# Optimization experiments

Measured on AMD Instinct MI355X. Metric: run time of the kernel, lower is better.

Reference implementation:

```python
import jax, jax.numpy as jnp
import numpy as np

N_USERS = 100000
EMBED = 128
N_EDGES = 1_600_000  # avg degree 16


def setup_inputs() -> dict:
    key = jax.random.key(0)
    k1, k2, k3, k4, k5 = jax.random.split(key, 5)
    s_rows = jnp.sort(jax.random.randint(k1, (N_EDGES,), 0, N_USERS))
    s_cols = jax.random.randint(k2, (N_EDGES,), 0, N_USERS)
    # row-normalization D^-1 A, matching the scipy preprocessing in __init__
    deg = jax.ops.segment_sum(jnp.ones((N_EDGES,), jnp.float32), s_rows, num_segments=N_USERS)
    deg = jnp.where(deg == 0, 1.0, deg)
    s_values = 1.0 / deg[s_rows]
    user_embeds = jax.random.normal(k3, (N_USERS, EMBED), jnp.float32) * 0.1
    bound = float(np.sqrt(6.0 / (EMBED + EMBED)))  # xavier_uniform
    W0 = jax.random.uniform(k4, (EMBED, EMBED), jnp.float32, -bound, bound)
    W1 = jax.random.uniform(k5, (EMBED, EMBED), jnp.float32, -bound, bound)
    return {"user_embeds": user_embeds, "s_rows": s_rows, "s_cols": s_cols,
            "s_values": s_values, "W0": W0, "W1": W1}


def reference(user_embeds, s_rows, s_cols, s_values, W0, W1):
    # SocialGCN.forward: per layer x_new = x + dropout(S @ (x @ W_l));
    # dropout is identity in eval mode. Returns all layer outputs (stacked).
    n_users = user_embeds.shape[0]
    outs = [user_embeds]
    x = user_embeds
    for W in (W0, W1):
        xt = x @ W  # [n_users, d] dense GEMM
        # SpMM: out[r] = sum_{e: rows[e]==r} vals[e] * xt[cols[e]]
        msg = s_values[:, None] * xt[s_cols]  # [n_edges, d] irregular gather
        agg = jax.ops.segment_sum(msg, s_rows, num_segments=n_users)
        x = x + agg  # residual add
        outs.append(x)
    return jnp.stack(outs)  # [n_layers+1, n_users, d]
```

## Files before the change

### kernel.cpp

```cpp
#include <hip/hip_runtime.h>

#define N_USERS  100000
#define EMBED    128

typedef __attribute__((ext_vector_type(8))) short bf16x8;
typedef __attribute__((ext_vector_type(4))) float f32x4;

__global__ __launch_bounds__(256) void rowptr_kernel(const int* __restrict__ rows,
                                                     int* __restrict__ row_ptr,
                                                     int n_rows, int n_edges) {
  int r = blockIdx.x * blockDim.x + threadIdx.x;
  if (r > n_rows) return;
  int lo = 0, hi = n_edges;
  while (lo < hi) {
    int mid = (lo + hi) >> 1;
    if (rows[mid] < r) lo = mid + 1; else hi = mid;
  }
  row_ptr[r] = lo;
}

__global__ __launch_bounds__(256) void wconv_kernel(const float* __restrict__ W0,
                                                    const float* __restrict__ W1,
                                                    uint* __restrict__ Wt0,
                                                    uint* __restrict__ Wt1) {
  const float* W  = blockIdx.x ? W1 : W0;
  uint*        Wt = blockIdx.x ? Wt1 : Wt0;
  for (int idx = threadIdx.x; idx < 128 * 64; idx += 256) {
    int n = idx >> 6;
    int kp = idx & 63;
    float a = W[(2 * kp) * 128 + n];
    float b = W[(2 * kp + 1) * 128 + n];
    uint o;
    asm("v_cvt_pk_bf16_f32 %0, %1, %2" : "=v"(o) : "v"(a), "v"(b));
    Wt[n * 64 + kp] = o;
  }
}

__global__ __launch_bounds__(256) void gemm_kernel(const float* __restrict__ X,
                                                   const ushort* __restrict__ Wt,
                                                   unsigned char* __restrict__ Y8,
                                                   float* __restrict__ scale_arr,
                                                   float* __restrict__ Xcopy) {
  const int tid  = threadIdx.x;
  const int wave = tid >> 6;
  const int lane = tid & 63;
  const int l15  = lane & 15;
  const int lg   = lane >> 4;
  const int m    = blockIdx.x * 64 + wave * 16 + l15;
  const int mc   = m < N_USERS ? m : N_USERS - 1;
  const bool act = m < N_USERS;
  const float* xrow = X + (size_t)mc * EMBED;

  f32x4 acc[8];
  #pragma unroll
  for (int t = 0; t < 8; ++t) acc[t] = (f32x4){0.f, 0.f, 0.f, 0.f};

  #pragma unroll
  for (int s = 0; s < 4; ++s) {
    const int k0 = s * 32 + lg * 8;
    float4 xa = *(const float4*)(xrow + k0);
    float4 xb = *(const float4*)(xrow + k0 + 4);
    if (Xcopy && act) {
      *(float4*)(Xcopy + (size_t)m * EMBED + k0)     = xa;
      *(float4*)(Xcopy + (size_t)m * EMBED + k0 + 4) = xb;
    }
    union { bf16x8 v; uint u[4]; } bfr;
    asm("v_cvt_pk_bf16_f32 %0, %1, %2" : "=v"(bfr.u[0]) : "v"(xa.x), "v"(xa.y));
    asm("v_cvt_pk_bf16_f32 %0, %1, %2" : "=v"(bfr.u[1]) : "v"(xa.z), "v"(xa.w));
    asm("v_cvt_pk_bf16_f32 %0, %1, %2" : "=v"(bfr.u[2]) : "v"(xb.x), "v"(xb.y));
    asm("v_cvt_pk_bf16_f32 %0, %1, %2" : "=v"(bfr.u[3]) : "v"(xb.z), "v"(xb.w));
    #pragma unroll
    for (int nt = 0; nt < 8; ++nt) {
      union { bf16x8 v; uint4 u; } afr;
      afr.u = *(const uint4*)(Wt + (size_t)(nt * 16 + l15) * 128 + k0);
      acc[nt] = __builtin_amdgcn_mfma_f32_16x16x32_bf16(afr.v, bfr.v, acc[nt], 0, 0, 0);
    }
  }

  if (act) {
    float amax = 0.f;
    #pragma unroll
    for (int nt = 0; nt < 8; ++nt)
      #pragma unroll
      for (int i = 0; i < 4; ++i) amax = fmaxf(amax, fabsf(acc[nt][i]));
    amax = fmaxf(amax, __shfl_xor(amax, 16));
    amax = fmaxf(amax, __shfl_xor(amax, 32));
    const float inv = amax > 0.f ? 127.0f / amax : 0.f;
    if (lg == 0) scale_arr[m] = amax * (1.0f / 127.0f);

    unsigned char* yrow = Y8 + (size_t)m * EMBED;
    #pragma unroll
    for (int nt = 0; nt < 8; ++nt) {
      uint q = 0;
      #pragma unroll
      for (int i = 0; i < 4; ++i) {
        int qi = __float2int_rn(acc[nt][i] * inv) + 128;
        q |= (uint)qi << (8 * i);
      }
      *(uint*)(yrow + nt * 16 + lg * 4) = q;
    }
  }
}

__device__ __forceinline__ void fma8b(float* a, uint2 g, float vs) {
  float f;
  #define CVT_ACC(word, b, slot)                                        \
    asm("v_cvt_f32_ubyte" #b " %0, %1" : "=v"(f) : "v"(word));          \
    a[slot] = fmaf(vs, f, a[slot]);
  CVT_ACC(g.x, 0, 0) CVT_ACC(g.x, 1, 1) CVT_ACC(g.x, 2, 2) CVT_ACC(g.x, 3, 3)
  CVT_ACC(g.y, 0, 4) CVT_ACC(g.y, 1, 5) CVT_ACC(g.y, 2, 6) CVT_ACC(g.y, 3, 7)
  #undef CVT_ACC
}

__global__ __launch_bounds__(256) void spmm_fused_kernel(
    const unsigned char* __restrict__ XT8, const float* __restrict__ scale_in,
    const float* __restrict__ X, const int* __restrict__ row_ptr,
    const int* __restrict__ cols, const float* __restrict__ vals,
    const ushort* __restrict__ Wt, float* __restrict__ OUT,
    unsigned char* __restrict__ Y8, float* __restrict__ scale_out) {
  const int tid  = threadIdx.x;
  const int wave = tid >> 6;
  const int lane = tid & 63;
  const int l15  = lane & 15;
  const int lg   = lane >> 4;
  const int row  = blockIdx.x * 64 + wave * 16 + l15;
  const int rowc = row < N_USERS ? row : N_USERS - 1;
  const bool act = row < N_USERS;
  const int start = row_ptr[rowc];
  const int end   = row_ptr[rowc + 1];

  float acc[4][8];
  #pragma unroll
  for (int s = 0; s < 4; ++s)
    #pragma unroll
    for (int j = 0; j < 8; ++j) acc[s][j] = 0.f;
  float vsum = 0.f;

  const uint2* base2 = (const uint2*)XT8;
  int e = start;
  int e_pre = (start + 3) & ~3;
  if (e_pre > end) e_pre = end;
  for (; e < e_pre; ++e) {
    int c = cols[e];
    float vs = vals[e] * scale_in[c];
    vsum += vs;
    const uint2* src = base2 + (size_t)c * 16 + lg;
    uint2 g0 = src[0], g1 = src[4], g2 = src[8], g3 = src[12];
    fma8b(acc[0], g0, vs); fma8b(acc[1], g1, vs);
    fma8b(acc[2], g2, vs); fma8b(acc[3], g3, vs);
  }
  for (; e + 4 <= end; e += 4) {
    int4   ca = *(const int4*)(cols + e);
    float4 va = *(const float4*)(vals + e);
    float vs0 = va.x * scale_in[ca.x], vs1 = va.y * scale_in[ca.y];
    float vs2 = va.z * scale_in[ca.z], vs3 = va.w * scale_in[ca.w];
    vsum += vs0 + vs1 + vs2 + vs3;
    const uint2* s0 = base2 + (size_t)ca.x * 16 + lg;
    const uint2* s1 = base2 + (size_t)ca.y * 16 + lg;
    const uint2* s2 = base2 + (size_t)ca.z * 16 + lg;
    const uint2* s3 = base2 + (size_t)ca.w * 16 + lg;
    uint2 a0 = s0[0], a1 = s0[4], a2 = s0[8],  a3 = s0[12];
    uint2 b0 = s1[0], b1 = s1[4], b2 = s1[8],  b3 = s1[12];
    uint2 c0 = s2[0], c1 = s2[4], c2 = s2[8],  c3 = s2[12];
    uint2 d0 = s3[0], d1 = s3[4], d2 = s3[8],  d3 = s3[12];
    fma8b(acc[0], a0, vs0); fma8b(acc[1], a1, vs0);
    fma8b(acc[2], a2, vs0); fma8b(acc[3], a3, vs0);
    fma8b(acc[0], b0, vs1); fma8b(acc[1], b1, vs1);
    fma8b(acc[2], b2, vs1); fma8b(acc[3], b3, vs1);
    fma8b(acc[0], c0, vs2); fma8b(acc[1], c1, vs2);
    fma8b(acc[2], c2, vs2); fma8b(acc[3], c3, vs2);
    fma8b(acc[0], d0, vs3); fma8b(acc[1], d1, vs3);
    fma8b(acc[2], d2, vs3); fma8b(acc[3], d3, vs3);
  }
  for (; e < end; ++e) {
    int c = cols[e];
    float vs = vals[e] * scale_in[c];
    vsum += vs;
    const uint2* src = base2 + (size_t)c * 16 + lg;
    uint2 g0 = src[0], g1 = src[4], g2 = src[8], g3 = src[12];
    fma8b(acc[0], g0, vs); fma8b(acc[1], g1, vs);
    fma8b(acc[2], g2, vs); fma8b(acc[3], g3, vs);
  }

  const float corr = vsum * 128.0f;
  union { bf16x8 v; uint4 u; } bfr[4];
  #pragma unroll
  for (int s = 0; s < 4; ++s) {
    const float* xr = X + (size_t)rowc * EMBED + s * 32 + lg * 8;
    float4 ra = *(const float4*)xr;
    float4 rb = *(const float4*)(xr + 4);
    float o0 = acc[s][0] - corr + ra.x, o1 = acc[s][1] - corr + ra.y;
    float o2 = acc[s][2] - corr + ra.z, o3 = acc[s][3] - corr + ra.w;
    float o4 = acc[s][4] - corr + rb.x, o5 = acc[s][5] - corr + rb.y;
    float o6 = acc[s][6] - corr + rb.z, o7 = acc[s][7] - corr + rb.w;
    if (act) {
      float* orow = OUT + (size_t)row * EMBED + s * 32 + lg * 8;
      *(float4*)orow       = (float4){o0, o1, o2, o3};
      *(float4*)(orow + 4) = (float4){o4, o5, o6, o7};
    }
    asm("v_cvt_pk_bf16_f32 %0, %1, %2" : "=v"(bfr[s].u.x) : "v"(o0), "v"(o1));
    asm("v_cvt_pk_bf16_f32 %0, %1, %2" : "=v"(bfr[s].u.y) : "v"(o2), "v"(o3));
    asm("v_cvt_pk_bf16_f32 %0, %1, %2" : "=v"(bfr[s].u.z) : "v"(o4), "v"(o5));
    asm("v_cvt_pk_bf16_f32 %0, %1, %2" : "=v"(bfr[s].u.w) : "v"(o6), "v"(o7));
  }

  f32x4 accg[8];
  #pragma unroll
  for (int t = 0; t < 8; ++t) accg[t] = (f32x4){0.f, 0.f, 0.f, 0.f};
  #pragma unroll
  for (int s = 0; s < 4; ++s) {
    const int k0 = s * 32 + lg * 8;
    #pragma unroll
    for (int nt = 0; nt < 8; ++nt) {
      union { bf16x8 v; uint4 u; } afr;
      afr.u = *(const uint4*)(Wt + (size_t)(nt * 16 + l15) * 128 + k0);
      accg[nt] = __builtin_amdgcn_mfma_f32_16x16x32_bf16(afr.v, bfr[s].v, accg[nt], 0, 0, 0);
    }
  }

  if (act) {
    float amax = 0.f;
    #pragma unroll
    for (int nt = 0; nt < 8; ++nt)
      #pragma unroll
      for (int i = 0; i < 4; ++i) amax = fmaxf(amax, fabsf(accg[nt][i]));
    amax = fmaxf(amax, __shfl_xor(amax, 16));
    amax = fmaxf(amax, __shfl_xor(amax, 32));
    const float inv = amax > 0.f ? 127.0f / amax : 0.f;
    if (lg == 0) scale_out[row] = amax * (1.0f / 127.0f);

    unsigned char* yrow = Y8 + (size_t)row * EMBED;
    #pragma unroll
    for (int nt = 0; nt < 8; ++nt) {
      uint q = 0;
      #pragma unroll
      for (int i = 0; i < 4; ++i) {
        int qi = __float2int_rn(accg[nt][i] * inv) + 128;
        q |= (uint)qi << (8 * i);
      }
      *(uint*)(yrow + nt * 16 + lg * 4) = q;
    }
  }
}

__device__ __forceinline__ void fma16(float* acc, uint4 g, float vs) {
  float f;
  #define CVT_ACC(word, b, slot)                                        \
    asm("v_cvt_f32_ubyte" #b " %0, %1" : "=v"(f) : "v"(word));          \
    acc[slot] = fmaf(vs, f, acc[slot]);
  CVT_ACC(g.x, 0, 0)  CVT_ACC(g.x, 1, 1)  CVT_ACC(g.x, 2, 2)  CVT_ACC(g.x, 3, 3)
  CVT_ACC(g.y, 0, 4)  CVT_ACC(g.y, 1, 5)  CVT_ACC(g.y, 2, 6)  CVT_ACC(g.y, 3, 7)
  CVT_ACC(g.z, 0, 8)  CVT_ACC(g.z, 1, 9)  CVT_ACC(g.z, 2, 10) CVT_ACC(g.z, 3, 11)
  CVT_ACC(g.w, 0, 12) CVT_ACC(g.w, 1, 13) CVT_ACC(g.w, 2, 14) CVT_ACC(g.w, 3, 15)
  #undef CVT_ACC
}

__global__ __launch_bounds__(256) void spmm_kernel(const unsigned char* __restrict__ XT8,
                                                   const float* __restrict__ scale_arr,
                                                   const float* __restrict__ X,
                                                   const int* __restrict__ row_ptr,
                                                   const int* __restrict__ cols,
                                                   const float* __restrict__ vals,
                                                   float* __restrict__ OUT) {
  const int tid = threadIdx.x;
  const int l   = tid & 7;
  const int rg  = tid >> 3;
  const int row = blockIdx.x * 32 + rg;
  if (row >= N_USERS) return;
  const int start = row_ptr[row];
  const int end   = row_ptr[row + 1];
  const uint4* XT4 = (const uint4*)XT8;

  float acc[16];
  #pragma unroll
  for (int j = 0; j < 16; ++j) acc[j] = 0.f;
  float vsum = 0.f;

  int e = start;
  int e_pre = (start + 3) & ~3;
  if (e_pre > end) e_pre = end;
  for (; e < e_pre; ++e) {
    int c = cols[e];
    float vs = vals[e] * scale_arr[c];
    vsum += vs;
    fma16(acc, XT4[(size_t)c * 8 + l], vs);
  }
  for (; e + 4 <= end; e += 4) {
    int4   ca = *(const int4*)(cols + e);
    float4 va = *(const float4*)(vals + e);
    float vs0 = va.x * scale_arr[ca.x], vs1 = va.y * scale_arr[ca.y];
    float vs2 = va.z * scale_arr[ca.z], vs3 = va.w * scale_arr[ca.w];
    uint4 g0 = XT4[(size_t)ca.x * 8 + l];
    uint4 g1 = XT4[(size_t)ca.y * 8 + l];
    uint4 g2 = XT4[(size_t)ca.z * 8 + l];
    uint4 g3 = XT4[(size_t)ca.w * 8 + l];
    vsum += vs0 + vs1 + vs2 + vs3;
    fma16(acc, g0, vs0);
    fma16(acc, g1, vs1);
    fma16(acc, g2, vs2);
    fma16(acc, g3, vs3);
  }
  for (; e < end; ++e) {
    int c = cols[e];
    float vs = vals[e] * scale_arr[c];
    vsum += vs;
    fma16(acc, XT4[(size_t)c * 8 + l], vs);
  }

  const float corr = vsum * 128.0f;
  const float* xr = X + (size_t)row * EMBED + l * 16;
  float*       orow = OUT + (size_t)row * EMBED + l * 16;
  #pragma unroll
  for (int k = 0; k < 4; ++k) {
    float4 r = *(const float4*)(xr + k * 4);
    float4 o = {acc[k * 4 + 0] - corr + r.x,
                acc[k * 4 + 1] - corr + r.y,
                acc[k * 4 + 2] - corr + r.z,
                acc[k * 4 + 3] - corr + r.w};
    *(float4*)(orow + k * 4) = o;
  }
}

extern "C" void kernel_launch(void* const* d_in, const int* in_sizes, int n_in,
                              void* d_out, int out_size, void* d_ws, size_t ws_size,
                              hipStream_t stream) {
  const float* user_embeds = (const float*)d_in[0];
  const int*   s_rows      = (const int*)d_in[1];
  const int*   s_cols      = (const int*)d_in[2];
  const float* s_values    = (const float*)d_in[3];
  const float* W0          = (const float*)d_in[4];
  const float* W1          = (const float*)d_in[5];
  float* out = (float*)d_out;

  const int n_edges = in_sizes[1];
  const size_t layer = (size_t)N_USERS * EMBED;

  char* ws = (char*)d_ws;
  unsigned char* xt8a = (unsigned char*)ws;  ws += layer;
  unsigned char* xt8b = (unsigned char*)ws;  ws += layer;
  float*  scale_a = (float*)ws;              ws += N_USERS * sizeof(float);
  float*  scale_b = (float*)ws;              ws += N_USERS * sizeof(float);
  ushort* Wt0     = (ushort*)ws;             ws += 128 * 128 * sizeof(ushort);
  ushort* Wt1     = (ushort*)ws;             ws += 128 * 128 * sizeof(ushort);
  int*    row_ptr = (int*)ws;

  rowptr_kernel<<<(N_USERS + 1 + 255) / 256, 256, 0, stream>>>(
      s_rows, row_ptr, N_USERS, n_edges);
  wconv_kernel<<<2, 256, 0, stream>>>(W0, W1, (uint*)Wt0, (uint*)Wt1);

  gemm_kernel<<<(N_USERS + 63) / 64, 256, 0, stream>>>(
      user_embeds, Wt0, xt8a, scale_a, out);
  spmm_fused_kernel<<<(N_USERS + 63) / 64, 256, 0, stream>>>(
      xt8a, scale_a, user_embeds, row_ptr, s_cols, s_values, Wt1,
      out + layer, xt8b, scale_b);
  spmm_kernel<<<(N_USERS + 31) / 32, 256, 0, stream>>>(
      xt8b, scale_b, out + layer, row_ptr, s_cols, s_values, out + 2 * layer);
}
```

Baseline: 226.5 us.

## Permute int8 embedding layout so SpMM gathers use 16-byte loads

The quantized XT8 rows are now written in a permuted order, so each lane in the fused SpMM kernel reads its 32 bytes per neighbor with two contiguous uint4 loads instead of four strided uint2 loads. The consumer kernels (fused and final SpMM) are updated to map output columns to that permuted layout. The fused kernel also reuses one accumulator union for both the aggregation and the MFMA stages and adds a min-blocks occupancy hint of 4. This aims to cut gather instruction count and register pressure, with the risk that any layout mismatch between writers and readers produces wrong results.

```diff
diff --git a/kernel.cpp b/kernel.cpp
--- a/kernel.cpp
+++ b/kernel.cpp
@@ -5,6 +5,7 @@
 
 typedef __attribute__((ext_vector_type(8))) short bf16x8;
 typedef __attribute__((ext_vector_type(4))) float f32x4;
+
 
 __global__ __launch_bounds__(256) void rowptr_kernel(const int* __restrict__ rows,
                                                      int* __restrict__ row_ptr,
@@ -88,7 +89,7 @@
     const float inv = amax > 0.f ? 127.0f / amax : 0.f;
     if (lg == 0) scale_arr[m] = amax * (1.0f / 127.0f);
 
-    unsigned char* yrow = Y8 + (size_t)m * EMBED;
+    uint* yrow = (uint*)(Y8 + (size_t)m * EMBED);
     #pragma unroll
     for (int nt = 0; nt < 8; ++nt) {
       uint q = 0;
@@ -97,22 +98,22 @@
         int qi = __float2int_rn(acc[nt][i] * inv) + 128;
         q |= (uint)qi << (8 * i);
       }
-      *(uint*)(yrow + nt * 16 + lg * 4) = q;
-    }
-  }
-}
-
-__device__ __forceinline__ void fma8b(float* a, uint2 g, float vs) {
+      yrow[(((nt & 1) << 1) | (lg >> 1)) * 8 + (nt >> 1) * 2 + (lg & 1)] = q;
+    }
+  }
+}
+
+__device__ __forceinline__ void fma8b(float* a, uint w0, uint w1, float vs) {
   float f;
   #define CVT_ACC(word, b, slot)                                        \
     asm("v_cvt_f32_ubyte" #b " %0, %1" : "=v"(f) : "v"(word));          \
     a[slot] = fmaf(vs, f, a[slot]);
-  CVT_ACC(g.x, 0, 0) CVT_ACC(g.x, 1, 1) CVT_ACC(g.x, 2, 2) CVT_ACC(g.x, 3, 3)
-  CVT_ACC(g.y, 0, 4) CVT_ACC(g.y, 1, 5) CVT_ACC(g.y, 2, 6) CVT_ACC(g.y, 3, 7)
+  CVT_ACC(w0, 0, 0) CVT_ACC(w0, 1, 1) CVT_ACC(w0, 2, 2) CVT_ACC(w0, 3, 3)
+  CVT_ACC(w1, 0, 4) CVT_ACC(w1, 1, 5) CVT_ACC(w1, 2, 6) CVT_ACC(w1, 3, 7)
   #undef CVT_ACC
 }
 
-__global__ __launch_bounds__(256) void spmm_fused_kernel(
+__global__ __launch_bounds__(256, 4) void spmm_fused_kernel(
     const unsigned char* __restrict__ XT8, const float* __restrict__ scale_in,
     const float* __restrict__ X, const int* __restrict__ row_ptr,
     const int* __restrict__ cols, const float* __restrict__ vals,
@@ -129,14 +130,12 @@
   const int start = row_ptr[rowc];
   const int end   = row_ptr[rowc + 1];
 
-  float acc[4][8];
-  #pragma unroll
-  for (int s = 0; s < 4; ++s)
-    #pragma unroll
-    for (int j = 0; j < 8; ++j) acc[s][j] = 0.f;
+  union AccU { float f[4][8]; f32x4 v[8]; } U;
+  #pragma unroll
+  for (int t = 0; t < 8; ++t) U.v[t] = (f32x4){0.f, 0.f, 0.f, 0.f};
   float vsum = 0.f;
 
-  const uint2* base2 = (const uint2*)XT8;
+  const uint4* B8 = (const uint4*)XT8;
   int e = start;
   int e_pre = (start + 3) & ~3;
   if (e_pre > end) e_pre = end;
@@ -144,10 +143,10 @@
     int c = cols[e];
     float vs = vals[e] * scale_in[c];
     vsum += vs;
-    const uint2* src = base2 + (size_t)c * 16 + lg;
-    uint2 g0 = src[0], g1 = src[4], g2 = src[8], g3 = src[12];
-    fma8b(acc[0], g0, vs); fma8b(acc[1], g1, vs);
-    fma8b(acc[2], g2, vs); fma8b(acc[3], g3, vs);
+    uint4 ga = B8[(size_t)c * 8 + lg * 2];
+    uint4 gb = B8[(size_t)c * 8 + lg * 2 + 1];
+    fma8b(U.f[0], ga.x, ga.y, vs); fma8b(U.f[1], ga.z, ga.w, vs);
+    fma8b(U.f[2], gb.x, gb.y, vs); fma8b(U.f[3], gb.z, gb.w, vs);
   }
   for (; e + 4 <= end; e += 4) {
     int4   ca = *(const int4*)(cols + e);
@@ -155,31 +154,27 @@
     float vs0 = va.x * scale_in[ca.x], vs1 = va.y * scale_in[ca.y];
     float vs2 = va.z * scale_in[ca.z], vs3 = va.w * scale_in[ca.w];
     vsum += vs0 + vs1 + vs2 + vs3;
-    const uint2* s0 = base2 + (size_t)ca.x * 16 + lg;
-    const uint2* s1 = base2 + (size_t)ca.y * 16 + lg;
-    const uint2* s2 = base2 + (size_t)ca.z * 16 + lg;
-    const uint2* s3 = base2 + (size_t)ca.w * 16 + lg;
-    uint2 a0 = s0[0], a1 = s0[4], a2 = s0[8],  a3 = s0[12];
-    uint2 b0 = s1[0], b1 = s1[4], b2 = s1[8],  b3 = s1[12];
-    uint2 c0 = s2[0], c1 = s2[4], c2 = s2[8],  c3 = s2[12];
-    uint2 d0 = s3[0], d1 = s3[4], d2 = s3[8],  d3 = s3[12];
-    fma8b(acc[0], a0, vs0); fma8b(acc[1], a1, vs0);
-    fma8b(acc[2], a2, vs0); fma8b(acc[3], a3, vs0);
-    fma8b(acc[0], b0, vs1); fma8b(acc[1], b1, vs1);
-    fma8b(acc[2], b2, vs1); fma8b(acc[3], b3, vs1);
-    fma8b(acc[0], c0, vs2); fma8b(acc[1], c1, vs2);
-    fma8b(acc[2], c2, vs2); fma8b(acc[3], c3, vs2);
-    fma8b(acc[0], d0, vs3); fma8b(acc[1], d1, vs3);
-    fma8b(acc[2], d2, vs3); fma8b(acc[3], d3, vs3);
+    uint4 a0 = B8[(size_t)ca.x * 8 + lg * 2], a1 = B8[(size_t)ca.x * 8 + lg * 2 + 1];
+    uint4 b0 = B8[(size_t)ca.y * 8 + lg * 2], b1 = B8[(size_t)ca.y * 8 + lg * 2 + 1];
+    uint4 c0 = B8[(size_t)ca.z * 8 + lg * 2], c1 = B8[(size_t)ca.z * 8 + lg * 2 + 1];
+    uint4 d0 = B8[(size_t)ca.w * 8 + lg * 2], d1 = B8[(size_t)ca.w * 8 + lg * 2 + 1];
+    fma8b(U.f[0], a0.x, a0.y, vs0); fma8b(U.f[1], a0.z, a0.w, vs0);
+    fma8b(U.f[2], a1.x, a1.y, vs0); fma8b(U.f[3], a1.z, a1.w, vs0);
+    fma8b(U.f[0], b0.x, b0.y, vs1); fma8b(U.f[1], b0.z, b0.w, vs1);
+    fma8b(U.f[2], b1.x, b1.y, vs1); fma8b(U.f[3], b1.z, b1.w, vs1);
+    fma8b(U.f[0], c0.x, c0.y, vs2); fma8b(U.f[1], c0.z, c0.w, vs2);
+    fma8b(U.f[2], c1.x, c1.y, vs2); fma8b(U.f[3], c1.z, c1.w, vs2);
+    fma8b(U.f[0], d0.x, d0.y, vs3); fma8b(U.f[1], d0.z, d0.w, vs3);
+    fma8b(U.f[2], d1.x, d1.y, vs3); fma8b(U.f[3], d1.z, d1.w, vs3);
   }
   for (; e < end; ++e) {
     int c = cols[e];
     float vs = vals[e] * scale_in[c];
     vsum += vs;
-    const uint2* src = base2 + (size_t)c * 16 + lg;
-    uint2 g0 = src[0], g1 = src[4], g2 = src[8], g3 = src[12];
-    fma8b(acc[0], g0, vs); fma8b(acc[1], g1, vs);
-    fma8b(acc[2], g2, vs); fma8b(acc[3], g3, vs);
+    uint4 ga = B8[(size_t)c * 8 + lg * 2];
+    uint4 gb = B8[(size_t)c * 8 + lg * 2 + 1];
+    fma8b(U.f[0], ga.x, ga.y, vs); fma8b(U.f[1], ga.z, ga.w, vs);
+    fma8b(U.f[2], gb.x, gb.y, vs); fma8b(U.f[3], gb.z, gb.w, vs);
   }
 
   const float corr = vsum * 128.0f;
@@ -189,10 +184,10 @@
     const float* xr = X + (size_t)rowc * EMBED + s * 32 + lg * 8;
     float4 ra = *(const float4*)xr;
     float4 rb = *(const float4*)(xr + 4);
-    float o0 = acc[s][0] - corr + ra.x, o1 = acc[s][1] - corr + ra.y;
-    float o2 = acc[s][2] - corr + ra.z, o3 = acc[s][3] - corr + ra.w;
-    float o4 = acc[s][4] - corr + rb.x, o5 = acc[s][5] - corr + rb.y;
-    float o6 = acc[s][6] - corr + rb.z, o7 = acc[s][7] - corr + rb.w;
+    float o0 = U.f[s][0] - corr + ra.x, o1 = U.f[s][1] - corr + ra.y;
+    float o2 = U.f[s][2] - corr + ra.z, o3 = U.f[s][3] - corr + ra.w;
+    float o4 = U.f[s][4] - corr + rb.x, o5 = U.f[s][5] - corr + rb.y;
+    float o6 = U.f[s][6] - corr + rb.z, o7 = U.f[s][7] - corr + rb.w;
     if (act) {
       float* orow = OUT + (size_t)row * EMBED + s * 32 + lg * 8;
       *(float4*)orow       = (float4){o0, o1, o2, o3};
@@ -204,9 +199,8 @@
     asm("v_cvt_pk_bf16_f32 %0, %1, %2" : "=v"(bfr[s].u.w) : "v"(o6), "v"(o7));
   }
 
-  f32x4 accg[8];
-  #pragma unroll
-  for (int t = 0; t < 8; ++t) accg[t] = (f32x4){0.f, 0.f, 0.f, 0.f};
+  #pragma unroll
+  for (int t = 0; t < 8; ++t) U.v[t] = (f32x4){0.f, 0.f, 0.f, 0.f};
   #pragma unroll
   for (int s = 0; s < 4; ++s) {
     const int k0 = s * 32 + lg * 8;
@@ -214,7 +208,7 @@
     for (int nt = 0; nt < 8; ++nt) {
       union { bf16x8 v; uint4 u; } afr;
       afr.u = *(const uint4*)(Wt + (size_t)(nt * 16 + l15) * 128 + k0);
-      accg[nt] = __builtin_amdgcn_mfma_f32_16x16x32_bf16(afr.v, bfr[s].v, accg[nt], 0, 0, 0);
+      U.v[nt] = __builtin_amdgcn_mfma_f32_16x16x32_bf16(afr.v, bfr[s].v, U.v[nt], 0, 0, 0);
     }
   }
 
@@ -223,22 +217,22 @@
     #pragma unroll
     for (int nt = 0; nt < 8; ++nt)
       #pragma unroll
-      for (int i = 0; i < 4; ++i) amax = fmaxf(amax, fabsf(accg[nt][i]));
+      for (int i = 0; i < 4; ++i) amax = fmaxf(amax, fabsf(U.v[nt][i]));
     amax = fmaxf(amax, __shfl_xor(amax, 16));
     amax = fmaxf(amax, __shfl_xor(amax, 32));
     const float inv = amax > 0.f ? 127.0f / amax : 0.f;
     if (lg == 0) scale_out[row] = amax * (1.0f / 127.0f);
 
-    unsigned char* yrow = Y8 + (size_t)row * EMBED;
+    uint* yrow = (uint*)(Y8 + (size_t)row * EMBED);
     #pragma unroll
     for (int nt = 0; nt < 8; ++nt) {
       uint q = 0;
       #pragma unroll
       for (int i = 0; i < 4; ++i) {
-        int qi = __float2int_rn(accg[nt][i] * inv) + 128;
+        int qi = __float2int_rn(U.v[nt][i] * inv) + 128;
         q |= (uint)qi << (8 * i);
       }
-      *(uint*)(yrow + nt * 16 + lg * 4) = q;
+      yrow[(((nt & 1) << 1) | (lg >> 1)) * 8 + (nt >> 1) * 2 + (lg & 1)] = q;
     }
   }
 }
@@ -308,17 +302,21 @@
   }
 
   const float corr = vsum * 128.0f;
-  const float* xr = X + (size_t)row * EMBED + l * 16;
-  float*       orow = OUT + (size_t)row * EMBED + l * 16;
-  #pragma unroll
-  for (int k = 0; k < 4; ++k) {
-    float4 r = *(const float4*)(xr + k * 4);
-    float4 o = {acc[k * 4 + 0] - corr + r.x,
-                acc[k * 4 + 1] - corr + r.y,
-                acc[k * 4 + 2] - corr + r.z,
-                acc[k * 4 + 3] - corr + r.w};
-    *(float4*)(orow + k * 4) = o;
-  }
+  const int colA = (l & 1) * 64 + (l >> 1) * 8;
+  const float* xrA = X + (size_t)row * EMBED + colA;
+  float*       orA = OUT + (size_t)row * EMBED + colA;
+  float4 rA0 = *(const float4*)xrA;
+  float4 rA1 = *(const float4*)(xrA + 4);
+  float4 rB0 = *(const float4*)(xrA + 32);
+  float4 rB1 = *(const float4*)(xrA + 36);
+  *(float4*)orA        = (float4){acc[0] - corr + rA0.x,  acc[1] - corr + rA0.y,
+                                  acc[2] - corr + rA0.z,  acc[3] - corr + rA0.w};
+  *(float4*)(orA + 4)  = (float4){acc[4] - corr + rA1.x,  acc[5] - corr + rA1.y,
+                                  acc[6] - corr + rA1.z,  acc[7] - corr + rA1.w};
+  *(float4*)(orA + 32) = (float4){acc[8] - corr + rB0.x,  acc[9] - corr + rB0.y,
+                                  acc[10] - corr + rB0.z, acc[11] - corr + rB0.w};
+  *(float4*)(orA + 36) = (float4){acc[12] - corr + rB1.x, acc[13] - corr + rB1.y,
+                                  acc[14] - corr + rB1.z, acc[15] - corr + rB1.w};
 }
 
 extern "C" void kernel_launch(void* const* d_in, const int* in_sizes, int n_in,
```

After: 202.6 us. -10.6%, faster.
